# Performance work log

Measured on AMD Instinct MI355X. Metric: run time of the kernel, lower is better.

Reference implementation:

```python
import jax, jax.numpy as jnp
import numpy as np

N_NODES = 50000
N_EDGES = 10000
NNZ = 1600000
IN_DIM = 256
OUT_DIM = 128


def setup_inputs() -> dict:
    key = jax.random.key(0)
    k1, k2, k3, k4, k5 = jax.random.split(key, 5)
    X = jax.random.normal(k1, (N_NODES, IN_DIM), dtype=jnp.float32)
    theta = jax.random.normal(k2, (IN_DIM, OUT_DIM), dtype=jnp.float32) * (1.0 / np.sqrt(IN_DIM))
    bias = jax.random.normal(k3, (OUT_DIM,), dtype=jnp.float32) * 0.01
    node_idx = jax.random.randint(k4, (NNZ,), 0, N_NODES, dtype=jnp.int32)
    hyedge_idx = jax.random.randint(k5, (NNZ,), 0, N_EDGES, dtype=jnp.int32)
    return {
        "X": X,
        "theta": theta,
        "bias": bias,
        "node_idx": node_idx,
        "hyedge_idx": hyedge_idx,
        "num_nodes": N_NODES,
        "num_edges": N_EDGES,
    }


def reference(X, theta, bias, node_idx, hyedge_idx, num_nodes, num_edges):
    # Dense transform: [N, in] @ [in, out] -> [N, out]
    Xt = X @ theta
    # MA_v: vertex -> hyperedge aggregation (gather by node_idx, scatter_add by hyedge_idx)
    Y = jax.ops.segment_sum(Xt[node_idx], hyedge_idx, num_segments=num_edges)  # [M, out]
    # MA_e: hyperedge -> vertex aggregation (gather by hyedge_idx, scatter_add by node_idx)
    X_new = jax.ops.segment_sum(Y[hyedge_idx], node_idx, num_segments=num_nodes)  # [N, out]
    # U_v: bias add
    return X_new + bias
```

## Files before the change

kernel.cpp:

```cpp
#include <hip/hip_runtime.h>
#include <hip/hip_bf16.h>

#define NN 50000
#define NE 10000
#define KD 256
#define MD 128

#define NCAP 76

#define RNG 4
#define RDIV 12500
#define ERCAP 96

#define NB_E 313
#define NB_N 196
#define NBT  (NB_E + NB_N)
#define CCAP_E 5760
#define CCAP_N 8960

#define GEMM_BLKS ((NN + 127) / 128)
#define NCB 256
#define CPB 6272
#define RPT ((CPB + 511) / 512)

typedef __attribute__((ext_vector_type(8))) short short8;
typedef __attribute__((ext_vector_type(4))) float f32x4;

union ABfrag { short8 s; unsigned u[4]; };

__device__ inline unsigned pack_bf2(float a, float b) {
    __hip_bfloat162 h = __float22bfloat162_rn(make_float2(a, b));
    return *reinterpret_cast<unsigned*>(&h);
}

__device__ inline unsigned short bf16_1(float a) {
    __hip_bfloat16 h = __float2bfloat16(a);
    return *reinterpret_cast<unsigned short*>(&h);
}

__device__ inline float bf_lo(unsigned v) { return __uint_as_float(v << 16); }
__device__ inline float bf_hi(unsigned v) { return __uint_as_float(v & 0xffff0000u); }

__device__ inline void exscan_block(const int* __restrict__ cnt, int* __restrict__ lst,
                                    int n, int* buf, int tid) {
    int v = (tid < n) ? cnt[tid] : 0;
    buf[tid] = v;
    __syncthreads();
    #pragma unroll
    for (int s = 1; s < 512; s <<= 1) {
        int t = (tid >= s) ? buf[tid - s] : 0;
        __syncthreads();
        buf[tid] += t;
        __syncthreads();
    }
    if (tid < n) lst[tid] = buf[tid] - v;
    __syncthreads();
}

__global__ __launch_bounds__(256) void prep_theta(const float* __restrict__ Th,
                                                  unsigned short* __restrict__ tT) {
    int gid = blockIdx.x * 256 + threadIdx.x;
    int k = gid >> 7, c = gid & 127;
    tT[(size_t)c * KD + k] = bf16_1(Th[(size_t)k * MD + c]);
}

__global__ __launch_bounds__(512) void gemm_coarse(const float* __restrict__ X,
                                                   const unsigned short* __restrict__ tT,
                                                   unsigned short* __restrict__ XtU, int N,
                                                   const int* __restrict__ nidx,
                                                   const int* __restrict__ eidx,
                                                   int* __restrict__ ccur,
                                                   unsigned* __restrict__ coarse_e,
                                                   unsigned* __restrict__ coarse_n, int nnz) {
    __shared__ unsigned srt[CPB];
    __shared__ int cntE[NB_E], lstE[NB_E], gbE[NB_E];
    __shared__ int cntN[NB_N], lstN[NB_N], gbN[NB_N];
    const int tid = threadIdx.x;

    if (blockIdx.x >= NCB) {
        const int w  = tid >> 6;
        const int l  = tid & 63;
        const int lr = l & 15;
        const int lk = l >> 4;
        const int row0 = (blockIdx.x - NCB) * 128 + w * 16;
        const int row  = row0 + lr;

        f32x4 acc[8];
        #pragma unroll
        for (int ct = 0; ct < 8; ++ct) acc[ct] = (f32x4){0.f, 0.f, 0.f, 0.f};

        const short8* tTv = (const short8*)tT;
        #pragma unroll
        for (int ks = 0; ks < 8; ++ks) {
            ABfrag a;
            if (row < N) {
                const float* xp = X + (size_t)row * KD + ks * 32 + lk * 8;
                float4 v0 = *(const float4*)(xp);
                float4 v1 = *(const float4*)(xp + 4);
                a.u[0] = pack_bf2(v0.x, v0.y);
                a.u[1] = pack_bf2(v0.z, v0.w);
                a.u[2] = pack_bf2(v1.x, v1.y);
                a.u[3] = pack_bf2(v1.z, v1.w);
            } else {
                a.u[0] = a.u[1] = a.u[2] = a.u[3] = 0u;
            }
            #pragma unroll
            for (int ct = 0; ct < 8; ++ct) {
                ABfrag b;
                b.s = tTv[(size_t)(ct * 16 + lr) * 32 + ks * 4 + lk];
                acc[ct] = __builtin_amdgcn_mfma_f32_16x16x32_bf16(a.s, b.s, acc[ct], 0, 0, 0);
            }
        }

        #pragma unroll
        for (int ct = 0; ct < 8; ++ct) {
            #pragma unroll
            for (int i = 0; i < 4; ++i) {
                int r = row0 + lk * 4 + i;
                if (r < N) XtU[(size_t)r * MD + ct * 16 + lr] = bf16_1(acc[ct][i]);
            }
        }
        return;
    }

    const int cbid = blockIdx.x;
    int C  = (nnz + NCB - 1) / NCB;
    if (C > CPB) C = CPB;
    const int k0 = cbid * C;
    int k1 = k0 + C; if (k1 > nnz) k1 = nnz;
    const int nk = k1 - k0;

    for (int j = tid; j < NB_E; j += 512) cntE[j] = 0;
    for (int j = tid; j < NB_N; j += 512) cntN[j] = 0;
    __syncthreads();

    unsigned rr[RPT];
    #pragma unroll
    for (int it = 0; it < RPT; ++it) {
        int i = tid + it * 512;
        unsigned r = 0u;
        if (i < nk) {
            int e = eidx[k0 + i], n = nidx[k0 + i];
            r = ((unsigned)n << 14) | (unsigned)e;
            atomicAdd(&cntE[e >> 5], 1);
            atomicAdd(&cntN[n >> 8], 1);
        }
        rr[it] = r;
    }
    __syncthreads();

    exscan_block(cntE, lstE, NB_E, (int*)srt, tid);
    exscan_block(cntN, lstN, NB_N, (int*)srt, tid);
    for (int j = tid; j < NB_E; j += 512) {
        int c = cntE[j];
        gbE[j] = c ? atomicAdd(&ccur[j], c) : 0;
    }
    for (int j = tid; j < NB_N; j += 512) {
        int c = cntN[j];
        gbN[j] = c ? atomicAdd(&ccur[NB_E + j], c) : 0;
    }
    __syncthreads();
    for (int j = tid; j < NB_E; j += 512) cntE[j] = 0;
    for (int j = tid; j < NB_N; j += 512) cntN[j] = 0;
    __syncthreads();

    #pragma unroll
    for (int it = 0; it < RPT; ++it) {
        int i = tid + it * 512;
        if (i < nk) {
            unsigned r = rr[it];
            int b = (r & 0x3FFF) >> 5;
            int rk = atomicAdd(&cntE[b], 1);
            srt[lstE[b] + rk] = r;
        }
    }
    __syncthreads();
    for (int p = tid; p < nk; p += 512) {
        unsigned r = srt[p];
        int b = (r & 0x3FFF) >> 5;
        int g = gbE[b] + (p - lstE[b]);
        if (g < CCAP_E) coarse_e[(size_t)b * CCAP_E + g] = r;
    }
    __syncthreads();

    #pragma unroll
    for (int it = 0; it < RPT; ++it) {
        int i = tid + it * 512;
        if (i < nk) {
            unsigned r = rr[it];
            int b = (int)(r >> 14) >> 8;
            int rk = atomicAdd(&cntN[b], 1);
            srt[lstN[b] + rk] = r;
        }
    }
    __syncthreads();
    for (int p = tid; p < nk; p += 512) {
        unsigned r = srt[p];
        int b = (int)(r >> 14) >> 8;
        int g = gbN[b] + (p - lstN[b]);
        if (g < CCAP_N) coarse_n[(size_t)b * CCAP_N + g] = r;
    }
}

__global__ __launch_bounds__(512) void fine_group(const unsigned* __restrict__ coarse_e,
                                                  const unsigned* __restrict__ coarse_n,
                                                  const int* __restrict__ ccur,
                                                  unsigned short* __restrict__ e_slots,
                                                  int* __restrict__ e_cnt,
                                                  unsigned short* __restrict__ n_slots,
                                                  int* __restrict__ n_cnt) {
    __shared__ unsigned srt[CCAP_N];
    __shared__ int cnt[256], lst[256];
    const int tid = threadIdx.x;
    const int b = blockIdx.x;

    if (b < NB_E) {
        const unsigned* buf = coarse_e + (size_t)b * CCAP_E;
        int m = ccur[b]; if (m > CCAP_E) m = CCAP_E;

        for (int j = tid; j < 128; j += 512) cnt[j] = 0;
        __syncthreads();
        for (int i = tid; i < m; i += 512) {
            unsigned r = buf[i];
            int e = r & 0x3FFF;
            int n = (int)(r >> 14);
            atomicAdd(&cnt[((e & 31) << 2) | (n / RDIV)], 1);
        }
        __syncthreads();
        exscan_block(cnt, lst, 128, (int*)srt, tid);
        if (tid < 128) {
            int e = b * 32 + (tid >> 2);
            if (e < NE) {
                int c = cnt[tid]; if (c > ERCAP) c = ERCAP;
                e_cnt[e * RNG + (tid & 3)] = c;
            }
        }
        __syncthreads();
        for (int j = tid; j < 128; j += 512) cnt[j] = 0;
        __syncthreads();
        for (int i = tid; i < m; i += 512) {
            unsigned r = buf[i];
            int e = r & 0x3FFF;
            unsigned n = r >> 14;
            int li = ((e & 31) << 2) | ((int)n / RDIV);
            int rk = atomicAdd(&cnt[li], 1);
            srt[lst[li] + rk] = ((unsigned)li << 16) | n;
        }
        __syncthreads();
        for (int p = tid; p < m; p += 512) {
            unsigned v = srt[p];
            int li = (int)(v >> 16);
            int lr = p - lst[li];
            if (lr < ERCAP) {
                int e = b * 32 + (li >> 2);
                e_slots[((size_t)e * RNG + (li & 3)) * ERCAP + lr] = (unsigned short)(v & 0xFFFF);
            }
        }
    } else {
        const unsigned* buf = coarse_n + (size_t)(b - NB_E) * CCAP_N;
        int m = ccur[b]; if (m > CCAP_N) m = CCAP_N;

        for (int j = tid; j < 256; j += 512) cnt[j] = 0;
        __syncthreads();
        for (int i = tid; i < m; i += 512) {
            unsigned r = buf[i];
            atomicAdd(&cnt[(r >> 14) & 255], 1);
        }
        __syncthreads();
        exscan_block(cnt, lst, 256, (int*)srt, tid);
        if (tid < 256) {
            int g = (b - NB_E) * 256 + tid;
            if (g < NN) {
                int c = cnt[tid]; if (c > NCAP) c = NCAP;
                n_cnt[g] = c;
            }
        }
        __syncthreads();
        for (int j = tid; j < 256; j += 512) cnt[j] = 0;
        __syncthreads();
        for (int i = tid; i < m; i += 512) {
            unsigned r = buf[i];
            int k = (r >> 14) & 255;
            int rk = atomicAdd(&cnt[k], 1);
            srt[lst[k] + rk] = ((unsigned)k << 16) | (r & 0x3FFF);
        }
        __syncthreads();
        for (int p = tid; p < m; p += 512) {
            unsigned v = srt[p];
            int k = (int)(v >> 16);
            int lr = p - lst[k];
            if (lr < NCAP) {
                int g = (b - NB_E) * 256 + k;
                n_slots[(size_t)g * NCAP + lr] = (unsigned short)(v & 0x3FFF);
            }
        }
    }
}

__global__ __launch_bounds__(256) void agg_ve_partial(const unsigned* __restrict__ XtB,
                                                      const int* __restrict__ e_cnt,
                                                      const unsigned short* __restrict__ e_slots,
                                                      unsigned* __restrict__ P) {
    const int r = blockIdx.x & 3;
    const int g = blockIdx.x >> 2;
    int wave = g * 4 + (threadIdx.x >> 6);
    int l    = threadIdx.x & 63;
    if (wave >= NE) return;
    const int grp = l >> 3, sub = l & 7;
    int cnt = e_cnt[wave * RNG + r]; if (cnt > ERCAP) cnt = ERCAP;
    const unsigned short* slots = e_slots + ((size_t)wave * RNG + r) * ERCAP;
    const uint4* Xv = (const uint4*)XtB;

    float a[16];
    #pragma unroll
    for (int i = 0; i < 16; ++i) a[i] = 0.f;

    for (int c = 0; c < cnt; c += 64) {
        int m = cnt - c; if (m > 64) m = 64;
        int idx = (c + l < cnt) ? (int)slots[c + l] : 0;
        for (int j = 0; j < m; j += 8) {
            int mem = j + grp;
            bool valid = mem < m;
            int n = __shfl(idx, valid ? mem : 0);
            const uint4* row = Xv + (size_t)n * 16 + sub * 2;
            uint4 v0 = row[0];
            uint4 v1 = row[1];
            if (valid) {
                a[0]  += bf_lo(v0.x); a[1]  += bf_hi(v0.x);
                a[2]  += bf_lo(v0.y); a[3]  += bf_hi(v0.y);
                a[4]  += bf_lo(v0.z); a[5]  += bf_hi(v0.z);
                a[6]  += bf_lo(v0.w); a[7]  += bf_hi(v0.w);
                a[8]  += bf_lo(v1.x); a[9]  += bf_hi(v1.x);
                a[10] += bf_lo(v1.y); a[11] += bf_hi(v1.y);
                a[12] += bf_lo(v1.z); a[13] += bf_hi(v1.z);
                a[14] += bf_lo(v1.w); a[15] += bf_hi(v1.w);
            }
        }
    }
    #pragma unroll
    for (int i = 0; i < 16; ++i) {
        a[i] += __shfl_xor(a[i], 8);
        a[i] += __shfl_xor(a[i], 16);
        a[i] += __shfl_xor(a[i], 32);
    }
    if (l < 8) {
        uint4 o0 = make_uint4(pack_bf2(a[0],  a[1]),  pack_bf2(a[2],  a[3]),
                              pack_bf2(a[4],  a[5]),  pack_bf2(a[6],  a[7]));
        uint4 o1 = make_uint4(pack_bf2(a[8],  a[9]),  pack_bf2(a[10], a[11]),
                              pack_bf2(a[12], a[13]), pack_bf2(a[14], a[15]));
        uint4* prow = (uint4*)P + ((size_t)r * NE + wave) * 16 + sub * 2;
        prow[0] = o0;
        prow[1] = o1;
    }
}

__global__ __launch_bounds__(256) void reduce_y(const unsigned* __restrict__ P,
                                                unsigned* __restrict__ YB) {
    int gid = blockIdx.x * 256 + threadIdx.x;
    if (gid >= NE * 64) return;
    float a = 0.f, b = 0.f;
    #pragma unroll
    for (int r = 0; r < RNG; ++r) {
        unsigned v = P[(size_t)r * NE * 64 + gid];
        a += bf_lo(v);
        b += bf_hi(v);
    }
    YB[gid] = pack_bf2(a, b);
}

__global__ __launch_bounds__(256) void agg_ev(const unsigned* __restrict__ YB,
                                              const int* __restrict__ n_cnt,
                                              const unsigned short* __restrict__ n_slots,
                                              const float* __restrict__ bias,
                                              float* __restrict__ out) {
    int wave = blockIdx.x * 4 + (threadIdx.x >> 6);
    int l    = threadIdx.x & 63;
    if (wave >= NN) return;
    const int grp = l >> 3, sub = l & 7;
    int cnt = n_cnt[wave]; if (cnt > NCAP) cnt = NCAP;
    const unsigned short* slots = n_slots + (size_t)wave * NCAP;
    const uint4* Yv = (const uint4*)YB;

    float a[16];
    #pragma unroll
    for (int i = 0; i < 16; ++i) a[i] = 0.f;

    for (int c = 0; c < cnt; c += 64) {
        int m = cnt - c; if (m > 64) m = 64;
        int idx = (c + l < cnt) ? (int)slots[c + l] : 0;
        for (int j = 0; j < m; j += 8) {
            int mem = j + grp;
            bool valid = mem < m;
            int e = __shfl(idx, valid ? mem : 0);
            const uint4* row = Yv + (size_t)e * 16 + sub * 2;
            uint4 v0 = row[0];
            uint4 v1 = row[1];
            if (valid) {
                a[0]  += bf_lo(v0.x); a[1]  += bf_hi(v0.x);
                a[2]  += bf_lo(v0.y); a[3]  += bf_hi(v0.y);
                a[4]  += bf_lo(v0.z); a[5]  += bf_hi(v0.z);
                a[6]  += bf_lo(v0.w); a[7]  += bf_hi(v0.w);
                a[8]  += bf_lo(v1.x); a[9]  += bf_hi(v1.x);
                a[10] += bf_lo(v1.y); a[11] += bf_hi(v1.y);
                a[12] += bf_lo(v1.z); a[13] += bf_hi(v1.z);
                a[14] += bf_lo(v1.w); a[15] += bf_hi(v1.w);
            }
        }
    }
    #pragma unroll
    for (int i = 0; i < 16; ++i) {
        a[i] += __shfl_xor(a[i], 8);
        a[i] += __shfl_xor(a[i], 16);
        a[i] += __shfl_xor(a[i], 32);
    }
    if (l < 8) {
        float4* orow = (float4*)(out + (size_t)wave * MD);
        #pragma unroll
        for (int q = 0; q < 4; ++q) {
            float4 bq = ((const float4*)bias)[sub * 4 + q];
            float4 o = make_float4(a[q * 4 + 0] + bq.x, a[q * 4 + 1] + bq.y,
                                   a[q * 4 + 2] + bq.z, a[q * 4 + 3] + bq.w);
            orow[sub * 4 + q] = o;
        }
    }
}

extern "C" void kernel_launch(void* const* d_in, const int* in_sizes, int n_in,
                              void* d_out, int out_size, void* d_ws, size_t ws_size,
                              hipStream_t stream) {
    const float* X     = (const float*)d_in[0];
    const float* theta = (const float*)d_in[1];
    const float* bias  = (const float*)d_in[2];
    const int*   nidx  = (const int*)d_in[3];
    const int*   eidx  = (const int*)d_in[4];
    float*       out   = (float*)d_out;

    const int N   = in_sizes[0] / KD;
    const int nnz = in_sizes[3];

    char* w = (char*)d_ws;
    unsigned*       XtB      = (unsigned*)w;       w += (size_t)NN * MD * 2;
    unsigned*       YB       = (unsigned*)w;       w += (size_t)NE * MD * 2;
    int*            e_cnt    = (int*)w;            w += (size_t)NE * RNG * 4;
    int*            n_cnt    = (int*)w;            w += (size_t)NN * 4;
    int*            ccur     = (int*)w;            w += (size_t)512 * 4;
    unsigned short* thetaT   = (unsigned short*)w; w += (size_t)MD * KD * 2;
    char*           uni      = w;
    unsigned*       coarse_e = (unsigned*)uni;
    unsigned*       coarse_n = (unsigned*)(uni + (size_t)NB_E * CCAP_E * 4);
    unsigned*       P        = (unsigned*)uni;
    {
        size_t coarse_sz = (size_t)NB_E * CCAP_E * 4 + (size_t)NB_N * CCAP_N * 4;
        size_t p_sz      = (size_t)RNG * NE * 64 * 4;
        w += (coarse_sz > p_sz) ? coarse_sz : p_sz;
    }
    unsigned short* e_slots  = (unsigned short*)w; w += (size_t)NE * RNG * ERCAP * 2;
    unsigned short* n_slots  = (unsigned short*)w;

    prep_theta<<<(MD * KD) / 256, 256, 0, stream>>>(theta, thetaT);
    hipMemsetAsync(ccur, 0, 512 * 4, stream);

    gemm_coarse<<<NCB + GEMM_BLKS, 512, 0, stream>>>(X, thetaT, (unsigned short*)XtB, N,
                                                     nidx, eidx, ccur,
                                                     coarse_e, coarse_n, nnz);

    fine_group<<<NBT, 512, 0, stream>>>(coarse_e, coarse_n, ccur,
                                        e_slots, e_cnt, n_slots, n_cnt);

    agg_ve_partial<<<(NE + 3) / 4 * RNG, 256, 0, stream>>>(XtB, e_cnt, e_slots, P);

    reduce_y<<<(NE * 64 + 255) / 256, 256, 0, stream>>>(P, YB);

    agg_ev<<<(NN + 3) / 4, 256, 0, stream>>>(YB, n_cnt, n_slots, bias, out);
}
```

Before: 138.6 us.

## Overlap node fine-grouping with vertex-to-edge aggregation and double GEMM rows per wave

Splits the fused fine-grouping kernel into an edge-only pass and a new kernel that runs node fine-grouping alongside the vertex-to-edge partial aggregation, so the node bucketing work overlaps with the gather phase instead of preceding it. The GEMM part now computes 32 rows per wave (two accumulator sets) to reuse each theta fragment load twice. The memset of counters is folded into the theta prep kernel, and the partial buffer P no longer aliases the coarse buffers so both can be live at once. This costs more workspace memory and more registers in the GEMM.

```diff
diff --git a/kernel.cpp b/kernel.cpp
--- a/kernel.cpp
+++ b/kernel.cpp
@@ -18,10 +18,12 @@
 #define CCAP_E 5760
 #define CCAP_N 8960
 
-#define GEMM_BLKS ((NN + 127) / 128)
+#define GEMM_BLKS ((NN + 255) / 256)
 #define NCB 256
 #define CPB 6272
 #define RPT ((CPB + 511) / 512)
+
+#define AGG_BLKS ((NE + 7) / 8 * RNG)
 
 typedef __attribute__((ext_vector_type(8))) short short8;
 typedef __attribute__((ext_vector_type(4))) float f32x4;
@@ -58,8 +60,11 @@
 }
 
 __global__ __launch_bounds__(256) void prep_theta(const float* __restrict__ Th,
-                                                  unsigned short* __restrict__ tT) {
-    int gid = blockIdx.x * 256 + threadIdx.x;
+                                                  unsigned short* __restrict__ tT,
+                                                  int* __restrict__ ccur) {
+    int tid = threadIdx.x;
+    if (blockIdx.x == 0) { ccur[tid] = 0; ccur[tid + 256] = 0; }
+    int gid = blockIdx.x * 256 + tid;
     int k = gid >> 7, c = gid & 127;
     tT[(size_t)c * KD + k] = bf16_1(Th[(size_t)k * MD + c]);
 }
@@ -82,33 +87,46 @@
         const int l  = tid & 63;
         const int lr = l & 15;
         const int lk = l >> 4;
-        const int row0 = (blockIdx.x - NCB) * 128 + w * 16;
-        const int row  = row0 + lr;
-
-        f32x4 acc[8];
+        const int row0 = (blockIdx.x - NCB) * 256 + w * 32;
+        const int rowA = row0 + lr;
+        const int rowB = row0 + 16 + lr;
+
+        f32x4 acc0[8], acc1[8];
         #pragma unroll
-        for (int ct = 0; ct < 8; ++ct) acc[ct] = (f32x4){0.f, 0.f, 0.f, 0.f};
+        for (int ct = 0; ct < 8; ++ct) {
+            acc0[ct] = (f32x4){0.f, 0.f, 0.f, 0.f};
+            acc1[ct] = (f32x4){0.f, 0.f, 0.f, 0.f};
+        }
 
         const short8* tTv = (const short8*)tT;
         #pragma unroll
         for (int ks = 0; ks < 8; ++ks) {
-            ABfrag a;
-            if (row < N) {
-                const float* xp = X + (size_t)row * KD + ks * 32 + lk * 8;
+            ABfrag a0, a1;
+            if (rowA < N) {
+                const float* xp = X + (size_t)rowA * KD + ks * 32 + lk * 8;
                 float4 v0 = *(const float4*)(xp);
                 float4 v1 = *(const float4*)(xp + 4);
-                a.u[0] = pack_bf2(v0.x, v0.y);
-                a.u[1] = pack_bf2(v0.z, v0.w);
-                a.u[2] = pack_bf2(v1.x, v1.y);
-                a.u[3] = pack_bf2(v1.z, v1.w);
-            } else {
-                a.u[0] = a.u[1] = a.u[2] = a.u[3] = 0u;
-            }
+                a0.u[0] = pack_bf2(v0.x, v0.y);
+                a0.u[1] = pack_bf2(v0.z, v0.w);
+                a0.u[2] = pack_bf2(v1.x, v1.y);
+                a0.u[3] = pack_bf2(v1.z, v1.w);
+            } else a0.u[0] = a0.u[1] = a0.u[2] = a0.u[3] = 0u;
+            if (rowB < N) {
+                const float* xp = X + (size_t)rowB * KD + ks * 32 + lk * 8;
+                float4 v0 = *(const float4*)(xp);
+                float4 v1 = *(const float4*)(xp + 4);
+                a1.u[0] = pack_bf2(v0.x, v0.y);
+                a1.u[1] = pack_bf2(v0.z, v0.w);
+                a1.u[2] = pack_bf2(v1.x, v1.y);
+                a1.u[3] = pack_bf2(v1.z, v1.w);
+            } else a1.u[0] = a1.u[1] = a1.u[2] = a1.u[3] = 0u;
+
             #pragma unroll
             for (int ct = 0; ct < 8; ++ct) {
                 ABfrag b;
                 b.s = tTv[(size_t)(ct * 16 + lr) * 32 + ks * 4 + lk];
-                acc[ct] = __builtin_amdgcn_mfma_f32_16x16x32_bf16(a.s, b.s, acc[ct], 0, 0, 0);
+                acc0[ct] = __builtin_amdgcn_mfma_f32_16x16x32_bf16(a0.s, b.s, acc0[ct], 0, 0, 0);
+                acc1[ct] = __builtin_amdgcn_mfma_f32_16x16x32_bf16(a1.s, b.s, acc1[ct], 0, 0, 0);
             }
         }
 
@@ -116,8 +134,10 @@
         for (int ct = 0; ct < 8; ++ct) {
             #pragma unroll
             for (int i = 0; i < 4; ++i) {
-                int r = row0 + lk * 4 + i;
-                if (r < N) XtU[(size_t)r * MD + ct * 16 + lr] = bf16_1(acc[ct][i]);
+                int rA = row0 + lk * 4 + i;
+                int rB = row0 + 16 + lk * 4 + i;
+                if (rA < N) XtU[(size_t)rA * MD + ct * 16 + lr] = bf16_1(acc0[ct][i]);
+                if (rB < N) XtU[(size_t)rB * MD + ct * 16 + lr] = bf16_1(acc1[ct][i]);
             }
         }
         return;
@@ -202,63 +222,74 @@
     }
 }
 
-__global__ __launch_bounds__(512) void fine_group(const unsigned* __restrict__ coarse_e,
-                                                  const unsigned* __restrict__ coarse_n,
-                                                  const int* __restrict__ ccur,
-                                                  unsigned short* __restrict__ e_slots,
-                                                  int* __restrict__ e_cnt,
-                                                  unsigned short* __restrict__ n_slots,
-                                                  int* __restrict__ n_cnt) {
+__global__ __launch_bounds__(512) void fine_e(const unsigned* __restrict__ coarse_e,
+                                              const int* __restrict__ ccur,
+                                              unsigned short* __restrict__ e_slots,
+                                              int* __restrict__ e_cnt) {
+    __shared__ unsigned srt[CCAP_E];
+    __shared__ int cnt[128], lst[128];
+    const int tid = threadIdx.x;
+    const int b = blockIdx.x;
+
+    const unsigned* buf = coarse_e + (size_t)b * CCAP_E;
+    int m = ccur[b]; if (m > CCAP_E) m = CCAP_E;
+
+    for (int j = tid; j < 128; j += 512) cnt[j] = 0;
+    __syncthreads();
+    for (int i = tid; i < m; i += 512) {
+        unsigned r = buf[i];
+        int e = r & 0x3FFF;
+        int n = (int)(r >> 14);
+        atomicAdd(&cnt[((e & 31) << 2) | (n / RDIV)], 1);
+    }
+    __syncthreads();
+    exscan_block(cnt, lst, 128, (int*)srt, tid);
+    if (tid < 128) {
+        int e = b * 32 + (tid >> 2);
+        if (e < NE) {
+            int c = cnt[tid]; if (c > ERCAP) c = ERCAP;
+            e_cnt[e * RNG + (tid & 3)] = c;
+        }
+    }
+    __syncthreads();
+    for (int j = tid; j < 128; j += 512) cnt[j] = 0;
+    __syncthreads();
+    for (int i = tid; i < m; i += 512) {
+        unsigned r = buf[i];
+        int e = r & 0x3FFF;
+        unsigned n = r >> 14;
+        int li = ((e & 31) << 2) | ((int)n / RDIV);
+        int rk = atomicAdd(&cnt[li], 1);
+        srt[lst[li] + rk] = ((unsigned)li << 16) | n;
+    }
+    __syncthreads();
+    for (int p = tid; p < m; p += 512) {
+        unsigned v = srt[p];
+        int li = (int)(v >> 16);
+        int lr = p - lst[li];
+        if (lr < ERCAP) {
+            int e = b * 32 + (li >> 2);
+            e_slots[((size_t)e * RNG + (li & 3)) * ERCAP + lr] = (unsigned short)(v & 0xFFFF);
+        }
+    }
+}
+
+__global__ __launch_bounds__(512) void fine_n_agg_ve(const unsigned* __restrict__ coarse_n,
+                                                     const int* __restrict__ ccur,
+                                                     unsigned short* __restrict__ n_slots,
+                                                     int* __restrict__ n_cnt,
+                                                     const unsigned* __restrict__ XtB,
+                                                     const int* __restrict__ e_cnt,
+                                                     const unsigned short* __restrict__ e_slots,
+                                                     unsigned* __restrict__ P) {
     __shared__ unsigned srt[CCAP_N];
     __shared__ int cnt[256], lst[256];
     const int tid = threadIdx.x;
-    const int b = blockIdx.x;
-
-    if (b < NB_E) {
-        const unsigned* buf = coarse_e + (size_t)b * CCAP_E;
-        int m = ccur[b]; if (m > CCAP_E) m = CCAP_E;
-
-        for (int j = tid; j < 128; j += 512) cnt[j] = 0;
-        __syncthreads();
-        for (int i = tid; i < m; i += 512) {
-            unsigned r = buf[i];
-            int e = r & 0x3FFF;
-            int n = (int)(r >> 14);
-            atomicAdd(&cnt[((e & 31) << 2) | (n / RDIV)], 1);
-        }
-        __syncthreads();
-        exscan_block(cnt, lst, 128, (int*)srt, tid);
-        if (tid < 128) {
-            int e = b * 32 + (tid >> 2);
-            if (e < NE) {
-                int c = cnt[tid]; if (c > ERCAP) c = ERCAP;
-                e_cnt[e * RNG + (tid & 3)] = c;
-            }
-        }
-        __syncthreads();
-        for (int j = tid; j < 128; j += 512) cnt[j] = 0;
-        __syncthreads();
-        for (int i = tid; i < m; i += 512) {
-            unsigned r = buf[i];
-            int e = r & 0x3FFF;
-            unsigned n = r >> 14;
-            int li = ((e & 31) << 2) | ((int)n / RDIV);
-            int rk = atomicAdd(&cnt[li], 1);
-            srt[lst[li] + rk] = ((unsigned)li << 16) | n;
-        }
-        __syncthreads();
-        for (int p = tid; p < m; p += 512) {
-            unsigned v = srt[p];
-            int li = (int)(v >> 16);
-            int lr = p - lst[li];
-            if (lr < ERCAP) {
-                int e = b * 32 + (li >> 2);
-                e_slots[((size_t)e * RNG + (li & 3)) * ERCAP + lr] = (unsigned short)(v & 0xFFFF);
-            }
-        }
-    } else {
-        const unsigned* buf = coarse_n + (size_t)(b - NB_E) * CCAP_N;
-        int m = ccur[b]; if (m > CCAP_N) m = CCAP_N;
+
+    if (blockIdx.x < NB_N) {
+        const int bb = blockIdx.x;
+        const unsigned* buf = coarse_n + (size_t)bb * CCAP_N;
+        int m = ccur[NB_E + bb]; if (m > CCAP_N) m = CCAP_N;
 
         for (int j = tid; j < 256; j += 512) cnt[j] = 0;
         __syncthreads();
@@ -269,7 +300,7 @@
         __syncthreads();
         exscan_block(cnt, lst, 256, (int*)srt, tid);
         if (tid < 256) {
-            int g = (b - NB_E) * 256 + tid;
+            int g = bb * 256 + tid;
             if (g < NN) {
                 int c = cnt[tid]; if (c > NCAP) c = NCAP;
                 n_cnt[g] = c;
@@ -290,24 +321,20 @@
             int k = (int)(v >> 16);
             int lr = p - lst[k];
             if (lr < NCAP) {
-                int g = (b - NB_E) * 256 + k;
+                int g = bb * 256 + k;
                 n_slots[(size_t)g * NCAP + lr] = (unsigned short)(v & 0x3FFF);
             }
         }
-    }
-}
-
-__global__ __launch_bounds__(256) void agg_ve_partial(const unsigned* __restrict__ XtB,
-                                                      const int* __restrict__ e_cnt,
-                                                      const unsigned short* __restrict__ e_slots,
-                                                      unsigned* __restrict__ P) {
-    const int r = blockIdx.x & 3;
-    const int g = blockIdx.x >> 2;
-    int wave = g * 4 + (threadIdx.x >> 6);
-    int l    = threadIdx.x & 63;
-    if (wave >= NE) return;
+        return;
+    }
+
+    const int wid = blockIdx.x - NB_N;
+    const int r = wid & 3;
+    const int g = wid >> 2;
+    int wave = g * 8 + (tid >> 6);
+    int l    = tid & 63;
     const int grp = l >> 3, sub = l & 7;
-    int cnt = e_cnt[wave * RNG + r]; if (cnt > ERCAP) cnt = ERCAP;
+    int ec = e_cnt[wave * RNG + r]; if (ec > ERCAP) ec = ERCAP;
     const unsigned short* slots = e_slots + ((size_t)wave * RNG + r) * ERCAP;
     const uint4* Xv = (const uint4*)XtB;
 
@@ -315,9 +342,9 @@
     #pragma unroll
     for (int i = 0; i < 16; ++i) a[i] = 0.f;
 
-    for (int c = 0; c < cnt; c += 64) {
-        int m = cnt - c; if (m > 64) m = 64;
-        int idx = (c + l < cnt) ? (int)slots[c + l] : 0;
+    for (int c = 0; c < ec; c += 64) {
+        int m = ec - c; if (m > 64) m = 64;
+        int idx = (c + l < ec) ? (int)slots[c + l] : 0;
         for (int j = 0; j < m; j += 8) {
             int mem = j + grp;
             bool valid = mem < m;
@@ -445,29 +472,22 @@
     int*            n_cnt    = (int*)w;            w += (size_t)NN * 4;
     int*            ccur     = (int*)w;            w += (size_t)512 * 4;
     unsigned short* thetaT   = (unsigned short*)w; w += (size_t)MD * KD * 2;
-    char*           uni      = w;
-    unsigned*       coarse_e = (unsigned*)uni;
-    unsigned*       coarse_n = (unsigned*)(uni + (size_t)NB_E * CCAP_E * 4);
-    unsigned*       P        = (unsigned*)uni;
-    {
-        size_t coarse_sz = (size_t)NB_E * CCAP_E * 4 + (size_t)NB_N * CCAP_N * 4;
-        size_t p_sz      = (size_t)RNG * NE * 64 * 4;
-        w += (coarse_sz > p_sz) ? coarse_sz : p_sz;
-    }
+    unsigned*       P        = (unsigned*)w;       w += (size_t)RNG * NE * 64 * 4;
+    unsigned*       coarse_e = (unsigned*)w;       w += (size_t)NB_E * CCAP_E * 4;
+    unsigned*       coarse_n = (unsigned*)w;       w += (size_t)NB_N * CCAP_N * 4;
     unsigned short* e_slots  = (unsigned short*)w; w += (size_t)NE * RNG * ERCAP * 2;
     unsigned short* n_slots  = (unsigned short*)w;
 
-    prep_theta<<<(MD * KD) / 256, 256, 0, stream>>>(theta, thetaT);
-    hipMemsetAsync(ccur, 0, 512 * 4, stream);
+    prep_theta<<<(MD * KD) / 256, 256, 0, stream>>>(theta, thetaT, ccur);
 
     gemm_coarse<<<NCB + GEMM_BLKS, 512, 0, stream>>>(X, thetaT, (unsigned short*)XtB, N,
                                                      nidx, eidx, ccur,
                                                      coarse_e, coarse_n, nnz);
 
-    fine_group<<<NBT, 512, 0, stream>>>(coarse_e, coarse_n, ccur,
-                                        e_slots, e_cnt, n_slots, n_cnt);
-
-    agg_ve_partial<<<(NE + 3) / 4 * RNG, 256, 0, stream>>>(XtB, e_cnt, e_slots, P);
+    fine_e<<<NB_E, 512, 0, stream>>>(coarse_e, ccur, e_slots, e_cnt);
+
+    fine_n_agg_ve<<<NB_N + AGG_BLKS, 512, 0, stream>>>(coarse_n, ccur, n_slots, n_cnt,
+                                                       XtB, e_cnt, e_slots, P);
 
     reduce_y<<<(NE * 64 + 255) / 256, 256, 0, stream>>>(P, YB);
 
```

New measurement: 126.3 us. 1.1x faster.
